# Optimization experiments

Measured on AMD Instinct MI355X. Metric: run time of the kernel, lower is better.

The kernel has to match this reference:

```python
import jax, jax.numpy as jnp
import numpy as np

B, H, S_MAX, D = 2, 32, 8192, 128
S_NEW = 512

def setup_inputs() -> dict:
    key = jax.random.key(0)
    k1, k2 = jax.random.split(key)
    return {
        "input_pos": jnp.arange(S_NEW, dtype=jnp.int64 if jax.config.jax_enable_x64 else jnp.int32),
        "k_val": jax.random.normal(k1, (B, H, S_NEW, D), dtype=jnp.float32),
        "v_val": jax.random.normal(k2, (B, H, S_NEW, D), dtype=jnp.float32),
        "k_cache": jnp.zeros((B, H, S_MAX, D), dtype=jnp.float32),
        "kt_cache": jnp.zeros((B, H, D, S_MAX), dtype=jnp.float32),
        "v_cache": jnp.zeros((B, H, S_MAX, D), dtype=jnp.float32),
    }

def reference(input_pos, k_val, v_val, k_cache, kt_cache, v_cache):
    # Scatter-write new K/V (and K^T) into the caches at input_pos.
    k_out = k_cache.at[:, :, input_pos].set(k_val)                      # [B,H,S_max,D]
    kt_out = kt_cache.at[:, :, :, input_pos].set(
        jnp.swapaxes(k_val, -1, -2))                                    # [B,H,D,S_max]
    v_out = v_cache.at[:, :, input_pos].set(v_val)                      # [B,H,S_max,D]
    # Module returns (kt.transpose(-1,-2), k, v)
    return (jnp.swapaxes(kt_out, -1, -2), k_out, v_out)
```

## Files before the change

kernel.cpp:

```cpp
#include <hip/hip_runtime.h>


#define S_MAXC 8192
#define DC     128
#define BHC    64

typedef __attribute__((ext_vector_type(4))) float v4f;

__global__ void init_inv(int* __restrict__ inv) {
    int i = blockIdx.x * blockDim.x + threadIdx.x;
    if (i < S_MAXC) inv[i] = -1;
}

__global__ void scatter_inv(const int* __restrict__ pos, int* __restrict__ inv, int n) {
    int j = blockIdx.x * blockDim.x + threadIdx.x;
    if (j < n) inv[pos[j]] = j;
}

__global__ void __launch_bounds__(256) fused_kv(
        const v4f* __restrict__ k_val,
        const v4f* __restrict__ v_val,
        const v4f* __restrict__ k_cache,
        const v4f* __restrict__ v_cache,
        const float* __restrict__ kt_cache,
        const int*  __restrict__ inv,
        v4f* __restrict__ out0,
        v4f* __restrict__ out1,
        v4f* __restrict__ out2,
        int s_new) {
    __shared__ __align__(16) float tile[32][132];
    const int tid = blockIdx.x;
    const int bh  = tid >> 8;
    const int s0  = (tid & 255) << 5;
    const int t   = threadIdx.x;
    const int q   = t & 7;
    const int r   = t >> 3;

    const float* ktb = kt_cache + (long)bh * DC * S_MAXC;
    #pragma unroll
    for (int p = 0; p < 4; ++p) {
        int d = p * 32 + r;
        v4f vld = __builtin_nontemporal_load(
            (const v4f*)(ktb + (long)d * S_MAXC + s0 + 4 * q));
        tile[4 * q + 0][d] = vld.x;
        tile[4 * q + 1][d] = vld.y;
        tile[4 * q + 2][d] = vld.z;
        tile[4 * q + 3][d] = vld.w;
    }
    __syncthreads();

    const int s = s0 + r;
    const int j = inv[s];
    const long row = (long)bh * S_MAXC + s;
    v4f* o0 = out0 + row * 32;
    v4f* o1 = out1 + row * 32;
    v4f* o2 = out2 + row * 32;
    if (j >= 0) {
        const v4f* kv = k_val + ((long)bh * s_new + j) * 32;
        const v4f* vv = v_val + ((long)bh * s_new + j) * 32;
        #pragma unroll
        for (int m = 0; m < 4; ++m) {
            int c = q + 8 * m;
            v4f kx = kv[c];
            v4f vx = vv[c];
            __builtin_nontemporal_store(kx, o0 + c);
            __builtin_nontemporal_store(kx, o1 + c);
            __builtin_nontemporal_store(vx, o2 + c);
        }
    } else {
        const v4f* kc = k_cache + row * 32;
        const v4f* vc = v_cache + row * 32;
        #pragma unroll
        for (int m = 0; m < 4; ++m) {
            int c = q + 8 * m;
            v4f kx = __builtin_nontemporal_load(kc + c);
            v4f vx = __builtin_nontemporal_load(vc + c);
            v4f tx = *(const v4f*)&tile[r][4 * c];
            __builtin_nontemporal_store(tx, o0 + c);
            __builtin_nontemporal_store(kx, o1 + c);
            __builtin_nontemporal_store(vx, o2 + c);
        }
    }
}

extern "C" void kernel_launch(void* const* d_in, const int* in_sizes, int n_in,
                              void* d_out, int out_size, void* d_ws, size_t ws_size,
                              hipStream_t stream) {
    const int*   input_pos = (const int*)  d_in[0];
    const float* k_val     = (const float*)d_in[1];
    const float* v_val     = (const float*)d_in[2];
    const float* k_cache   = (const float*)d_in[3];
    const float* kt_cache  = (const float*)d_in[4];
    const float* v_cache   = (const float*)d_in[5];
    const int s_new = in_sizes[0];

    const long per_out = (long)BHC * S_MAXC * DC;
    float* out0 = (float*)d_out;
    float* out1 = out0 + per_out;
    float* out2 = out1 + per_out;

    int* inv = (int*)d_ws;

    init_inv<<<S_MAXC / 256, 256, 0, stream>>>(inv);
    scatter_inv<<<(s_new + 255) / 256, 256, 0, stream>>>(input_pos, inv, s_new);

    const int n_tiles = BHC * (S_MAXC / 32);
    fused_kv<<<n_tiles, 256, 0, stream>>>(
        (const v4f*)k_val, (const v4f*)v_val,
        (const v4f*)k_cache, (const v4f*)v_cache,
        kt_cache, inv,
        (v4f*)out0, (v4f*)out1, (v4f*)out2, s_new);
}
```

Measured before the change: 1.253 ms.

## Merge inverse-index kernels, enlarge transpose tile, swizzle LDS, stage index in shared

```diff
diff --git a/kernel.cpp b/kernel.cpp
--- a/kernel.cpp
+++ b/kernel.cpp
@@ -4,20 +4,20 @@
 #define S_MAXC 8192
 #define DC     128
 #define BHC    64
+#define TS     64
+#define NTHR   512
 
 typedef __attribute__((ext_vector_type(4))) float v4f;
 
-__global__ void init_inv(int* __restrict__ inv) {
-    int i = blockIdx.x * blockDim.x + threadIdx.x;
-    if (i < S_MAXC) inv[i] = -1;
+__global__ void build_inv(const int* __restrict__ pos, int* __restrict__ inv, int n) {
+    const int t = threadIdx.x;
+    #pragma unroll
+    for (int i = t; i < S_MAXC; i += NTHR) inv[i] = -1;
+    __syncthreads();
+    for (int j = t; j < n; j += NTHR) inv[pos[j]] = j;
 }
 
-__global__ void scatter_inv(const int* __restrict__ pos, int* __restrict__ inv, int n) {
-    int j = blockIdx.x * blockDim.x + threadIdx.x;
-    if (j < n) inv[pos[j]] = j;
-}
-
-__global__ void __launch_bounds__(256) fused_kv(
+__global__ void __launch_bounds__(NTHR) fused_kv(
         const v4f* __restrict__ k_val,
         const v4f* __restrict__ v_val,
         const v4f* __restrict__ k_cache,
@@ -28,57 +28,61 @@
         v4f* __restrict__ out1,
         v4f* __restrict__ out2,
         int s_new) {
-    __shared__ __align__(16) float tile[32][132];
-    const int tid = blockIdx.x;
-    const int bh  = tid >> 8;
-    const int s0  = (tid & 255) << 5;
+    __shared__ __align__(16) float tile[TS][132];
+    __shared__ int linv[TS];
+
+    const int blk = blockIdx.x;
+    const int bh  = blk >> 7;
+    const int s0  = (blk & 127) << 6;
     const int t   = threadIdx.x;
-    const int q   = t & 7;
-    const int r   = t >> 3;
 
-    const float* ktb = kt_cache + (long)bh * DC * S_MAXC;
-    #pragma unroll
-    for (int p = 0; p < 4; ++p) {
-        int d = p * 32 + r;
-        v4f vld = __builtin_nontemporal_load(
-            (const v4f*)(ktb + (long)d * S_MAXC + s0 + 4 * q));
-        tile[4 * q + 0][d] = vld.x;
-        tile[4 * q + 1][d] = vld.y;
-        tile[4 * q + 2][d] = vld.z;
-        tile[4 * q + 3][d] = vld.w;
+    if (t < TS) linv[t] = inv[s0 + t];
+
+    {
+        const float* ktb = kt_cache + (long)bh * (DC * S_MAXC);
+        const int q = t & 15;
+        const int r = t >> 4;
+        const int g = q & 7;
+        #pragma unroll
+        for (int p = 0; p < 4; ++p) {
+            const int d = (p << 5) | r;
+            v4f vld = __builtin_nontemporal_load(
+                (const v4f*)(ktb + (long)d * S_MAXC + s0 + (q << 2)));
+            const int dsw = ((((d >> 2) ^ g) << 2) | (d & 3));
+            tile[(q << 2) + 0][dsw] = vld.x;
+            tile[(q << 2) + 1][dsw] = vld.y;
+            tile[(q << 2) + 2][dsw] = vld.z;
+            tile[(q << 2) + 3][dsw] = vld.w;
+        }
     }
     __syncthreads();
 
-    const int s = s0 + r;
-    const int j = inv[s];
-    const long row = (long)bh * S_MAXC + s;
-    v4f* o0 = out0 + row * 32;
-    v4f* o1 = out1 + row * 32;
-    v4f* o2 = out2 + row * 32;
-    if (j >= 0) {
-        const v4f* kv = k_val + ((long)bh * s_new + j) * 32;
-        const v4f* vv = v_val + ((long)bh * s_new + j) * 32;
-        #pragma unroll
-        for (int m = 0; m < 4; ++m) {
-            int c = q + 8 * m;
-            v4f kx = kv[c];
-            v4f vx = vv[c];
-            __builtin_nontemporal_store(kx, o0 + c);
-            __builtin_nontemporal_store(kx, o1 + c);
-            __builtin_nontemporal_store(vx, o2 + c);
-        }
-    } else {
-        const v4f* kc = k_cache + row * 32;
-        const v4f* vc = v_cache + row * 32;
-        #pragma unroll
-        for (int m = 0; m < 4; ++m) {
-            int c = q + 8 * m;
-            v4f kx = __builtin_nontemporal_load(kc + c);
-            v4f vx = __builtin_nontemporal_load(vc + c);
-            v4f tx = *(const v4f*)&tile[r][4 * c];
-            __builtin_nontemporal_store(tx, o0 + c);
-            __builtin_nontemporal_store(kx, o1 + c);
-            __builtin_nontemporal_store(vx, o2 + c);
+    const int c  = t & 31;
+    const int tt = t >> 5;
+    #pragma unroll
+    for (int m = 0; m < 4; ++m) {
+        const int rl = (m << 4) | tt;
+        const int s  = s0 + rl;
+        const int j  = linv[rl];
+        const long row = (long)bh * S_MAXC + s;
+        v4f* o0 = out0 + row * 32 + c;
+        v4f* o1 = out1 + row * 32 + c;
+        v4f* o2 = out2 + row * 32 + c;
+        if (j >= 0) {
+            const long vrow = ((long)bh * s_new + j) * 32 + c;
+            v4f kx = k_val[vrow];
+            v4f vx = v_val[vrow];
+            __builtin_nontemporal_store(kx, o0);
+            __builtin_nontemporal_store(kx, o1);
+            __builtin_nontemporal_store(vx, o2);
+        } else {
+            v4f kx = __builtin_nontemporal_load(k_cache + row * 32 + c);
+            v4f vx = __builtin_nontemporal_load(v_cache + row * 32 + c);
+            const int g2 = (rl >> 2) & 7;
+            v4f tx = *(const v4f*)&tile[rl][(c ^ g2) << 2];
+            __builtin_nontemporal_store(tx, o0);
+            __builtin_nontemporal_store(kx, o1);
+            __builtin_nontemporal_store(vx, o2);
         }
     }
 }
@@ -101,11 +105,10 @@
 
     int* inv = (int*)d_ws;
 
-    init_inv<<<S_MAXC / 256, 256, 0, stream>>>(inv);
-    scatter_inv<<<(s_new + 255) / 256, 256, 0, stream>>>(input_pos, inv, s_new);
+    build_inv<<<1, NTHR, 0, stream>>>(input_pos, inv, s_new);
 
-    const int n_tiles = BHC * (S_MAXC / 32);
-    fused_kv<<<n_tiles, 256, 0, stream>>>(
+    const int n_tiles = BHC * (S_MAXC / TS);
+    fused_kv<<<n_tiles, NTHR, 0, stream>>>(
         (const v4f*)k_val, (const v4f*)v_val,
         (const v4f*)k_cache, (const v4f*)v_cache,
         kt_cache, inv,
```

After: 1.262 ms. Within noise of the previous version (+0.7%).
